# Performance work log

Measured on AMD Instinct MI355X. Metric: run time of the kernel, lower is better.

The kernel has to match this reference:

```python
import jax, jax.numpy as jnp
import numpy as np

HIDDEN = 2048
N_HEADS = 16
N_KV_GROUPS = 4
HEAD_DIM = HIDDEN // N_HEADS  # 128
LATENT = 512
KV_SIZE = HIDDEN * N_KV_GROUPS // N_HEADS  # 512


def setup_inputs() -> dict:
    key = jax.random.key(0)
    ks = jax.random.split(key, 11)
    s = 0.02
    return {
        "hidden_states": jax.random.normal(ks[0], (2, 2048, HIDDEN), dtype=jnp.float32),
        "Wq": jax.random.normal(ks[1], (HIDDEN, HIDDEN), dtype=jnp.float32) * s,
        "bq": jnp.zeros((HIDDEN,), dtype=jnp.float32),
        "Wl": jax.random.normal(ks[2], (HIDDEN, LATENT), dtype=jnp.float32) * s,
        "bl": jnp.zeros((LATENT,), dtype=jnp.float32),
        "Wk": jax.random.normal(ks[3], (LATENT, KV_SIZE), dtype=jnp.float32) * s,
        "bk": jnp.zeros((KV_SIZE,), dtype=jnp.float32),
        "Wv": jax.random.normal(ks[4], (LATENT, KV_SIZE), dtype=jnp.float32) * s,
        "bv": jnp.zeros((KV_SIZE,), dtype=jnp.float32),
        "Wo": jax.random.normal(ks[5], (HIDDEN, HIDDEN), dtype=jnp.float32) * s,
        "bo": jnp.zeros((HIDDEN,), dtype=jnp.float32),
    }


def reference(hidden_states, Wq, bq, Wl, bl, Wk, bk, Wv, bv, Wo, bo):
    B, S, _ = hidden_states.shape
    heads_per_group = N_HEADS // N_KV_GROUPS

    q = hidden_states @ Wq + bq                      # [B,S,H*D]
    latent = hidden_states @ Wl + bl                 # [B,S,L]
    k = latent @ Wk + bk                             # [B,S,G*D]
    v = latent @ Wv + bv

    q = q.reshape(B, S, N_HEADS, HEAD_DIM).transpose(0, 2, 1, 3)        # [B,H,S,D]
    k = k.reshape(B, S, N_KV_GROUPS, HEAD_DIM).transpose(0, 2, 1, 3)    # [B,G,S,D]
    v = v.reshape(B, S, N_KV_GROUPS, HEAD_DIM).transpose(0, 2, 1, 3)

    # repeat_interleave over head dim: group g -> heads [g*hpg, (g+1)*hpg)
    k = jnp.repeat(k, heads_per_group, axis=1)       # [B,H,S,D]
    v = jnp.repeat(v, heads_per_group, axis=1)

    scale = 1.0 / np.sqrt(HEAD_DIM).astype(np.float32)
    scores = jnp.einsum("bhqd,bhkd->bhqk", q, k) * scale
    probs = jax.nn.softmax(scores, axis=-1)          # dropout p=0 (eval) -> identity
    ctx = jnp.einsum("bhqk,bhkd->bhqd", probs, v)    # [B,H,S,D]
    ctx = ctx.transpose(0, 2, 1, 3).reshape(B, S, HIDDEN)
    return ctx @ Wo + bo
```

## Files before the change

### kernel.cpp

```cpp
#include <hip/hip_runtime.h>
#include <stdint.h>


#define DEV static __device__ __forceinline__

using short8 = __attribute__((ext_vector_type(8))) short;
using f32x4  = __attribute__((ext_vector_type(4))) float;

typedef __attribute__((address_space(1))) void gvoid;
typedef __attribute__((address_space(3))) void lvoid;

DEV unsigned short f2b(float f) {
  unsigned u = __builtin_bit_cast(unsigned, f);
  unsigned r = (u + 0x7fffu + ((u >> 16) & 1u)) >> 16;
  return (unsigned short)r;
}
DEV float b2f(unsigned short s) {
  unsigned u = ((unsigned)s) << 16;
  return __builtin_bit_cast(float, u);
}

DEV unsigned cvtpk(float lo, float hi) {
  unsigned r;
  asm("v_cvt_pk_bf16_f32 %0, %1, %2" : "=v"(r) : "v"(lo), "v"(hi));
  return r;
}

DEV float ex2(float x) { return __builtin_amdgcn_exp2f(x); }

DEV void async16(const void* g, void* l) {
  __builtin_amdgcn_global_load_lds((gvoid*)(uintptr_t)g,
                                   (lvoid*)(uint32_t)(uintptr_t)l, 16, 0, 0);
}

DEV f32x4 mfma16(short8 a, short8 b, f32x4 c) {
  return __builtin_amdgcn_mfma_f32_16x16x32_bf16(a, b, c, 0, 0, 0);
}

__global__ __launch_bounds__(256) void mega_prep(
    const float* __restrict__ h, unsigned short* __restrict__ hb,
    const float* __restrict__ Wq, const float* __restrict__ Wl,
    const float* __restrict__ Wk, const float* __restrict__ Wv,
    const float* __restrict__ Wo,
    unsigned short* __restrict__ WqlT, unsigned short* __restrict__ WkvT,
    unsigned short* __restrict__ WoT,
    const float* __restrict__ bq, const float* __restrict__ bl,
    const float* __restrict__ bk, const float* __restrict__ bv,
    float* __restrict__ bql, float* __restrict__ bkv, float qscale) {
  __shared__ float tile[32][33];
  const int bid = blockIdx.x;
  const int tid = threadIdx.x;

  if (bid < 4096) {
    long i = ((long)bid * 256 + tid) * 8;
    float4 a = *(const float4*)(h + i);
    float4 b = *(const float4*)(h + i + 4);
    short8 o;
    o[0] = (short)f2b(a.x); o[1] = (short)f2b(a.y);
    o[2] = (short)f2b(a.z); o[3] = (short)f2b(a.w);
    o[4] = (short)f2b(b.x); o[5] = (short)f2b(b.y);
    o[6] = (short)f2b(b.z); o[7] = (short)f2b(b.w);
    *(short8*)(hb + i) = o;
    return;
  }

  const float* in; unsigned short* out; int R, C, bx, by; float sc = 1.0f;
  if (bid < 8192) {
    int l = bid - 4096; in = Wq; out = WqlT; R = 2048; C = 2048;
    bx = l & 63; by = l >> 6; sc = qscale;
  } else if (bid < 9216) {
    int l = bid - 8192; in = Wl; out = WqlT + 2048 * 2048; R = 2048; C = 512;
    bx = l & 15; by = l >> 4;
  } else if (bid < 9472) {
    int l = bid - 9216; in = Wk; out = WkvT; R = 512; C = 512;
    bx = l & 15; by = l >> 4;
  } else if (bid < 9728) {
    int l = bid - 9472; in = Wv; out = WkvT + 262144; R = 512; C = 512;
    bx = l & 15; by = l >> 4;
  } else if (bid < 13824) {
    int l = bid - 9728; in = Wo; out = WoT; R = 2048; C = 2048;
    bx = l & 63; by = l >> 6;
  } else {
    for (int t = tid; t < 2560; t += 256)
      bql[t] = (t < 2048) ? bq[t] * qscale : bl[t - 2048];
    for (int t = tid; t < 1024; t += 256)
      bkv[t] = (t < 512) ? bk[t] : bv[t - 512];
    return;
  }

  int bc = bx * 32, br = by * 32;
  int tx = tid & 31, ty0 = tid >> 5;
#pragma unroll
  for (int ty = ty0; ty < 32; ty += 8)
    tile[ty][tx] = in[(size_t)(br + ty) * C + bc + tx] * sc;
  __syncthreads();
#pragma unroll
  for (int ty = ty0; ty < 32; ty += 8)
    out[(size_t)(bc + ty) * R + br + tx] = f2b(tile[tx][ty]);
}

__global__ __launch_bounds__(256) void transpose_v(
    const unsigned short* __restrict__ in, unsigned short* __restrict__ out) {
  __shared__ float tile[32][33];
  int b = blockIdx.z;
  int bc = blockIdx.x * 32;
  int br = blockIdx.y * 32;
  const unsigned short* ip = in + (size_t)b * 2048 * 1024 + 512;
  unsigned short* op = out + (size_t)b * 512 * 2048;
  int tx = threadIdx.x & 31, ty0 = threadIdx.x >> 5;
#pragma unroll
  for (int ty = ty0; ty < 32; ty += 8)
    tile[ty][tx] = b2f(ip[(size_t)(br + ty) * 1024 + bc + tx]);
  __syncthreads();
#pragma unroll
  for (int ty = ty0; ty < 32; ty += 8)
    op[(size_t)(bc + ty) * 2048 + br + tx] = f2b(tile[tx][ty]);
}

template <int OUT_F32>
__global__ __launch_bounds__(256) void gemm_bt(
    const unsigned short* __restrict__ A, const unsigned short* __restrict__ Bt,
    const float* __restrict__ bias, void* __restrict__ Cout,
    int M, int N, int K, int lda, float scale) {
  __shared__ unsigned short As[128 * 32];
  __shared__ unsigned short Bs[128 * 32];
  int tid = threadIdx.x;
  int lane = tid & 63, wave = tid >> 6;
  int wr = wave >> 1, wc = wave & 1;
  int lq = lane & 15, grp = lane >> 4;
  int brow = blockIdx.y * 128, bcol = blockIdx.x * 128;

  f32x4 acc[4][4] = {};

  for (int k0 = 0; k0 < K; k0 += 32) {
    {
      int e0 = tid * 8;
      int r0 = e0 >> 5, c0 = e0 & 31;
      async16(A + (size_t)(brow + r0) * lda + k0 + c0, As + e0);
      async16(Bt + (size_t)(bcol + r0) * K + k0 + c0, Bs + e0);
      int e1 = (256 + tid) * 8;
      int r1 = e1 >> 5, c1 = e1 & 31;
      async16(A + (size_t)(brow + r1) * lda + k0 + c1, As + e1);
      async16(Bt + (size_t)(bcol + r1) * K + k0 + c1, Bs + e1);
    }
    __syncthreads();

    short8 af[4], bf[4];
#pragma unroll
    for (int m = 0; m < 4; m++)
      af[m] = *(const short8*)(As + (wr * 64 + m * 16 + lq) * 32 + grp * 8);
#pragma unroll
    for (int n = 0; n < 4; n++)
      bf[n] = *(const short8*)(Bs + (wc * 64 + n * 16 + lq) * 32 + grp * 8);
#pragma unroll
    for (int m = 0; m < 4; m++)
#pragma unroll
      for (int n = 0; n < 4; n++)
        acc[m][n] = mfma16(af[m], bf[n], acc[m][n]);
    __syncthreads();
  }

#pragma unroll
  for (int n = 0; n < 4; n++) {
    int col = bcol + wc * 64 + n * 16 + lq;
    float bv = bias[col];
#pragma unroll
    for (int m = 0; m < 4; m++) {
#pragma unroll
      for (int r = 0; r < 4; r++) {
        int row = brow + wr * 64 + m * 16 + grp * 4 + r;
        float v = (acc[m][n][r] + bv) * scale;
        if (OUT_F32)
          ((float*)Cout)[(size_t)row * N + col] = v;
        else
          ((unsigned short*)Cout)[(size_t)row * N + col] = f2b(v);
      }
    }
  }
}

template <int OUT_F32>
__global__ __launch_bounds__(512, 1) void gemm_8ph(
    const unsigned short* __restrict__ A, const unsigned short* __restrict__ Bt,
    const float* __restrict__ bias, void* __restrict__ Cout,
    int M, int N, int K, float scale) {
  __shared__ __align__(1024) unsigned short L[2][32768];
  const int tid = threadIdx.x, lane = tid & 63, wave = tid >> 6;
  const int lq = lane & 15, grp = lane >> 4;
  const int wr = wave >> 2, wc = wave & 3;

  const int gx = gridDim.x;
  int nwg = gx * gridDim.y;
  int bid = blockIdx.y * gx + blockIdx.x;
  int wgid = (bid & 7) * (nwg >> 3) + (bid >> 3);
  int bx = wgid % gx, by = wgid / gx;
  const int brow = by * 256, bcol = bx * 256;

  const unsigned short* srcA[2];
  const unsigned short* srcB[2];
  unsigned short* dstA[2];
  unsigned short* dstB[2];
#pragma unroll
  for (int j = 0; j < 2; j++) {
    int f = wave + j * 8, kk = f & 1, fi = f >> 1;
    int awr = fi >> 2, aml = fi & 3;
    srcA[j] = A + (size_t)(brow + (awr * 8 + aml) * 16 + lq) * K + kk * 32 + grp * 8;
    dstA[j] = &L[0][0] + f * 512 + lane * 8;
    int bwc = fi >> 1, bnl = fi & 1;
    srcB[j] = Bt + (size_t)(bcol + (bwc * 4 + bnl) * 16 + lq) * K + kk * 32 + grp * 8;
    dstB[j] = &L[0][0] + 16384 + f * 512 + lane * 8;
  }
  auto stgA = [&](int p, int mh, int k0) {
#pragma unroll
    for (int j = 0; j < 2; j++)
      async16(srcA[j] + (size_t)mh * 64 * K + k0, dstA[j] + p * 32768 + mh * 8192);
  };
  auto stgB = [&](int p, int nh, int k0) {
#pragma unroll
    for (int j = 0; j < 2; j++)
      async16(srcB[j] + (size_t)nh * 32 * K + k0, dstB[j] + p * 32768 + nh * 8192);
  };
  auto ldAf = [&](int p, int mh, int ml, int kk) -> short8 {
    return *(const short8*)(&L[0][0] + p * 32768 + mh * 8192 +
                            ((wr * 4 + ml) * 2 + kk) * 512 + lane * 8);
  };
  auto ldBf = [&](int p, int nh, int nl, int kk) -> short8 {
    return *(const short8*)(&L[0][0] + p * 32768 + 16384 + nh * 8192 +
                            ((wc * 2 + nl) * 2 + kk) * 512 + lane * 8);
  };

  f32x4 acc[8][4] = {};
  short8 af[4][2], bf0[2][2], bf1[2][2];
  const int NT = K >> 6;

  stgA(0, 0, 0); stgB(0, 0, 0); stgB(0, 1, 0); stgA(0, 1, 0);
  asm volatile("s_waitcnt vmcnt(4)" ::: "memory");
  __builtin_amdgcn_s_barrier();

  for (int T = 0; T < NT; ++T) {
    const int cur = T & 1, nxt = cur ^ 1;
    const bool pf = (T + 1 < NT);
    const int k1 = (T + 1) << 6;

#pragma unroll
    for (int ml = 0; ml < 4; ml++) {
      af[ml][0] = ldAf(cur, 0, ml, 0);
      af[ml][1] = ldAf(cur, 0, ml, 1);
    }
#pragma unroll
    for (int nl = 0; nl < 2; nl++) {
      bf0[nl][0] = ldBf(cur, 0, nl, 0);
      bf0[nl][1] = ldBf(cur, 0, nl, 1);
    }
    if (pf) stgA(nxt, 0, k1);
    __builtin_amdgcn_s_setprio(1);
#pragma unroll
    for (int ml = 0; ml < 4; ml++)
#pragma unroll
      for (int nl = 0; nl < 2; nl++) {
        acc[ml][nl] = mfma16(af[ml][0], bf0[nl][0], acc[ml][nl]);
        acc[ml][nl] = mfma16(af[ml][1], bf0[nl][1], acc[ml][nl]);
      }
    __builtin_amdgcn_s_setprio(0);
    if (pf) asm volatile("s_waitcnt vmcnt(4)" ::: "memory");
    else    asm volatile("s_waitcnt vmcnt(2)" ::: "memory");
    __builtin_amdgcn_s_barrier();

#pragma unroll
    for (int nl = 0; nl < 2; nl++) {
      bf1[nl][0] = ldBf(cur, 1, nl, 0);
      bf1[nl][1] = ldBf(cur, 1, nl, 1);
    }
    if (pf) stgB(nxt, 0, k1);
    __builtin_amdgcn_s_setprio(1);
#pragma unroll
    for (int ml = 0; ml < 4; ml++)
#pragma unroll
      for (int nl = 0; nl < 2; nl++) {
        acc[ml][2 + nl] = mfma16(af[ml][0], bf1[nl][0], acc[ml][2 + nl]);
        acc[ml][2 + nl] = mfma16(af[ml][1], bf1[nl][1], acc[ml][2 + nl]);
      }
    __builtin_amdgcn_s_setprio(0);
    if (pf) asm volatile("s_waitcnt vmcnt(4)" ::: "memory");
    else    asm volatile("s_waitcnt vmcnt(0)" ::: "memory");
    __builtin_amdgcn_s_barrier();

#pragma unroll
    for (int ml = 0; ml < 4; ml++) {
      af[ml][0] = ldAf(cur, 1, ml, 0);
      af[ml][1] = ldAf(cur, 1, ml, 1);
    }
    if (pf) stgB(nxt, 1, k1);
    __builtin_amdgcn_s_setprio(1);
#pragma unroll
    for (int ml = 0; ml < 4; ml++)
#pragma unroll
      for (int nl = 0; nl < 2; nl++) {
        acc[4 + ml][nl] = mfma16(af[ml][0], bf0[nl][0], acc[4 + ml][nl]);
        acc[4 + ml][nl] = mfma16(af[ml][1], bf0[nl][1], acc[4 + ml][nl]);
      }
    __builtin_amdgcn_s_setprio(0);
    __builtin_amdgcn_s_barrier();

    if (pf) stgA(nxt, 1, k1);
    __builtin_amdgcn_s_setprio(1);
#pragma unroll
    for (int ml = 0; ml < 4; ml++)
#pragma unroll
      for (int nl = 0; nl < 2; nl++) {
        acc[4 + ml][2 + nl] = mfma16(af[ml][0], bf1[nl][0], acc[4 + ml][2 + nl]);
        acc[4 + ml][2 + nl] = mfma16(af[ml][1], bf1[nl][1], acc[4 + ml][2 + nl]);
      }
    __builtin_amdgcn_s_setprio(0);
    if (pf) asm volatile("s_waitcnt vmcnt(4)" ::: "memory");
    __builtin_amdgcn_s_barrier();
  }

#pragma unroll
  for (int mh = 0; mh < 2; mh++)
#pragma unroll
    for (int ml = 0; ml < 4; ml++)
#pragma unroll
      for (int nh = 0; nh < 2; nh++)
#pragma unroll
        for (int nl = 0; nl < 2; nl++) {
          int col = bcol + wc * 64 + (nh * 2 + nl) * 16 + lq;
          float bv = bias[col];
          f32x4 a = acc[mh * 4 + ml][nh * 2 + nl];
#pragma unroll
          for (int r = 0; r < 4; r++) {
            int row = brow + wr * 128 + (mh * 4 + ml) * 16 + grp * 4 + r;
            float v = (a[r] + bv) * scale;
            if (OUT_F32)
              ((float*)Cout)[(size_t)row * N + col] = v;
            else
              ((unsigned short*)Cout)[(size_t)row * N + col] = f2b(v);
          }
        }
}

__global__ __launch_bounds__(256, 2) void attn_kernel(
    const unsigned short* __restrict__ q,
    const unsigned short* __restrict__ kv,
    const unsigned short* __restrict__ vt,
    unsigned short* __restrict__ ctx) {
  __shared__ unsigned short KV[2][32][512];
  const int lane = threadIdx.x & 63, wave = threadIdx.x >> 6;
  const int lq = lane & 15, grp = lane >> 4;
  const int bid = blockIdx.x;
  const int combo = bid & 7;
  const int slot = bid >> 3;
  const int b = combo >> 2, g = combo & 3;
  const int h = g * 4 + (slot >> 4);
  const int qbase = (slot & 15) * 128 + wave * 32;

  short8 qf[2][4];
#pragma unroll
  for (int qs = 0; qs < 2; qs++) {
    const unsigned short* qp =
        q + ((size_t)(b * 2048 + qbase + qs * 16 + lq)) * 2560 + h * 128 + grp * 8;
#pragma unroll
    for (int c = 0; c < 4; c++) qf[qs][c] = *(const short8*)(qp + c * 32);
  }

  f32x4 o[2][8] = {};
  float lsum[2] = {0.f, 0.f};
  const float C = 20.0f;

  const int kvperm = (lq >> 2) * 8 + (lq & 3);
  const unsigned short* kB = kv + (size_t)b * 2048 * 1024 + g * 128 + grp * 8;
  const unsigned short* vB =
      vt + ((size_t)((b * 4 + g) * 128 + lq)) * 2048 + grp * 8;
  const int fbase = wave * 8;
  unsigned short* dstb = &KV[0][fbase][0] + lane * 8;

  auto stage = [&](int bn, int kv0) {
    unsigned short* dst = dstb + bn * 16384;
    if (fbase < 16) {
#pragma unroll
      for (int j = 0; j < 8; j++) {
        int f = fbase + j, t = f >> 2, c = f & 3;
        const unsigned short* src =
            kB + (size_t)(kv0 + (t >> 1) * 32 + (t & 1) * 4 + kvperm) * 1024 + c * 32;
        async16(src, dst + j * 512);
      }
    } else {
#pragma unroll
      for (int j = 0; j < 8; j++) {
        int f = fbase - 16 + j, d0 = f >> 1, u = f & 1;
        const unsigned short* src = vB + (size_t)(d0 * 16) * 2048 + kv0 + u * 32;
        async16(src, dst + j * 512);
      }
    }
  };

  stage(0, 0);
  int buf = 0;
  for (int it = 0; it < 32; ++it) {
    __syncthreads();
    if (it < 31) stage(buf ^ 1, (it + 1) * 64);
    const unsigned short* Kb = &KV[buf][0][0] + lane * 8;

    f32x4 s[2][4] = {};
    __builtin_amdgcn_s_setprio(1);
#pragma unroll
    for (int c = 0; c < 4; c++) {
      short8 kf0 = *(const short8*)(Kb + (0 + c) * 512);
      short8 kf1 = *(const short8*)(Kb + (4 + c) * 512);
      short8 kf2 = *(const short8*)(Kb + (8 + c) * 512);
      short8 kf3 = *(const short8*)(Kb + (12 + c) * 512);
#pragma unroll
      for (int qs = 0; qs < 2; qs++) {
        s[qs][0] = mfma16(kf0, qf[qs][c], s[qs][0]);
        s[qs][1] = mfma16(kf1, qf[qs][c], s[qs][1]);
        s[qs][2] = mfma16(kf2, qf[qs][c], s[qs][2]);
        s[qs][3] = mfma16(kf3, qf[qs][c], s[qs][3]);
      }
    }
    __builtin_amdgcn_s_setprio(0);

    short8 pf[2][2];
#pragma unroll
    for (int qs = 0; qs < 2; qs++) {
      float ps = 0.f;
      union { short8 v; unsigned w[4]; } pk0, pk1;
#pragma unroll
      for (int t = 0; t < 4; t++) {
        float e0 = ex2(s[qs][t][0] - C);
        float e1 = ex2(s[qs][t][1] - C);
        float e2 = ex2(s[qs][t][2] - C);
        float e3 = ex2(s[qs][t][3] - C);
        ps += (e0 + e1) + (e2 + e3);
        unsigned w0 = cvtpk(e0, e1), w1 = cvtpk(e2, e3);
        if (t == 0) { pk0.w[0] = w0; pk0.w[1] = w1; }
        else if (t == 1) { pk0.w[2] = w0; pk0.w[3] = w1; }
        else if (t == 2) { pk1.w[0] = w0; pk1.w[1] = w1; }
        else { pk1.w[2] = w0; pk1.w[3] = w1; }
      }
      lsum[qs] += ps;
      pf[qs][0] = pk0.v;
      pf[qs][1] = pk1.v;
    }

    const unsigned short* Vb = Kb + 16 * 512;
    __builtin_amdgcn_s_setprio(1);
#pragma unroll
    for (int d0 = 0; d0 < 8; d0++) {
      short8 v0 = *(const short8*)(Vb + (d0 * 2 + 0) * 512);
      short8 v1 = *(const short8*)(Vb + (d0 * 2 + 1) * 512);
#pragma unroll
      for (int qs = 0; qs < 2; qs++) {
        o[qs][d0] = mfma16(pf[qs][0], v0, o[qs][d0]);
        o[qs][d0] = mfma16(pf[qs][1], v1, o[qs][d0]);
      }
    }
    __builtin_amdgcn_s_setprio(0);
    buf ^= 1;
  }

  unsigned short* cp = ctx + ((size_t)(b * 2048 + qbase)) * 2048 + h * 128;
#pragma unroll
  for (int qs = 0; qs < 2; qs++) {
    float l = lsum[qs];
    l += __shfl_xor(l, 16);
    l += __shfl_xor(l, 32);
    float ri = 1.0f / l;
    float r0 = __shfl(ri, grp * 4 + 0), r1 = __shfl(ri, grp * 4 + 1);
    float r2 = __shfl(ri, grp * 4 + 2), r3 = __shfl(ri, grp * 4 + 3);
#pragma unroll
    for (int d0 = 0; d0 < 8; d0++) {
      int col = d0 * 16 + lq;
      cp[(size_t)(qs * 16 + grp * 4 + 0) * 2048 + col] = f2b(o[qs][d0][0] * r0);
      cp[(size_t)(qs * 16 + grp * 4 + 1) * 2048 + col] = f2b(o[qs][d0][1] * r1);
      cp[(size_t)(qs * 16 + grp * 4 + 2) * 2048 + col] = f2b(o[qs][d0][2] * r2);
      cp[(size_t)(qs * 16 + grp * 4 + 3) * 2048 + col] = f2b(o[qs][d0][3] * r3);
    }
  }
}

extern "C" void kernel_launch(void* const* d_in, const int* in_sizes, int n_in,
                              void* d_out, int out_size, void* d_ws, size_t ws_size,
                              hipStream_t stream) {
  const float* h  = (const float*)d_in[0];
  const float* Wq = (const float*)d_in[1];
  const float* bq = (const float*)d_in[2];
  const float* Wl = (const float*)d_in[3];
  const float* bl = (const float*)d_in[4];
  const float* Wk = (const float*)d_in[5];
  const float* bk = (const float*)d_in[6];
  const float* Wv = (const float*)d_in[7];
  const float* bv = (const float*)d_in[8];
  const float* Wo = (const float*)d_in[9];
  const float* bo = (const float*)d_in[10];
  float* out = (float*)d_out;

  const int M = 4096;

  char* w = (char*)d_ws;
  auto take = [&](size_t elems) {
    void* p = (void*)w;
    w += (elems * 2 + 255) & ~(size_t)255;
    return (unsigned short*)p;
  };
  unsigned short* hb   = take(8388608);
  unsigned short* WqlT = take(5242880);
  unsigned short* WkvT = take(524288);
  unsigned short* WoT  = take(4194304);
  unsigned short* qlat = take(10485760);
  unsigned short* kvb  = take(4194304);
  unsigned short* vtb  = take(2097152);
  unsigned short* ctx  = take(8388608);
  float* bql = (float*)take(2560);
  float* bkv = (float*)take(1024);

  const float scale = 0.08838834764831845f * 1.4426950408889634f;

  mega_prep<<<13825, 256, 0, stream>>>(h, hb, Wq, Wl, Wk, Wv, Wo,
                                       WqlT, WkvT, WoT,
                                       bq, bl, bk, bv, bql, bkv, scale);

  gemm_8ph<0><<<dim3(10, 16), 512, 0, stream>>>(hb, WqlT, bql, qlat, M, 2560, 2048, 1.0f);
  gemm_bt<0><<<dim3(8, 32), 256, 0, stream>>>(qlat + 2048, WkvT, bkv, kvb, M, 1024, 512, 2560, 1.0f);

  transpose_v<<<dim3(16, 64, 2), 256, 0, stream>>>(kvb, vtb);

  attn_kernel<<<512, 256, 0, stream>>>(qlat, kvb, vtb, ctx);

  gemm_8ph<1><<<dim3(8, 16), 512, 0, stream>>>(ctx, WoT, bo, out, M, 2048, 2048, 1.0f);
}
```

Before: 241.5 us.

## Split fused Q/latent GEMM and switch to 256x128 two-phase GEMM tiles

Replaces the 256x256 eight-phase GEMM with a 256x128 tile kernel using two B sub-phases, giving 256 workgroups instead of 160/128 for the Q and output projections. The fused Q+latent projection is split into a separate Q GEMM and a latent GEMM run by the smaller gemm_bt kernel, so buffers and bias layouts change (q row stride becomes 2048). The goal is better CU fill on the 256-CU device, at the cost of lower per-tile reuse and one extra kernel launch.

```diff
diff --git a/kernel.cpp b/kernel.cpp
--- a/kernel.cpp
+++ b/kernel.cpp
@@ -42,11 +42,11 @@
     const float* __restrict__ Wq, const float* __restrict__ Wl,
     const float* __restrict__ Wk, const float* __restrict__ Wv,
     const float* __restrict__ Wo,
-    unsigned short* __restrict__ WqlT, unsigned short* __restrict__ WkvT,
-    unsigned short* __restrict__ WoT,
-    const float* __restrict__ bq, const float* __restrict__ bl,
+    unsigned short* __restrict__ WqT, unsigned short* __restrict__ WlT,
+    unsigned short* __restrict__ WkvT, unsigned short* __restrict__ WoT,
+    const float* __restrict__ bq,
     const float* __restrict__ bk, const float* __restrict__ bv,
-    float* __restrict__ bql, float* __restrict__ bkv, float qscale) {
+    float* __restrict__ bqs, float* __restrict__ bkv, float qscale) {
   __shared__ float tile[32][33];
   const int bid = blockIdx.x;
   const int tid = threadIdx.x;
@@ -66,10 +66,10 @@
 
   const float* in; unsigned short* out; int R, C, bx, by; float sc = 1.0f;
   if (bid < 8192) {
-    int l = bid - 4096; in = Wq; out = WqlT; R = 2048; C = 2048;
+    int l = bid - 4096; in = Wq; out = WqT; R = 2048; C = 2048;
     bx = l & 63; by = l >> 6; sc = qscale;
   } else if (bid < 9216) {
-    int l = bid - 8192; in = Wl; out = WqlT + 2048 * 2048; R = 2048; C = 512;
+    int l = bid - 8192; in = Wl; out = WlT; R = 2048; C = 512;
     bx = l & 15; by = l >> 4;
   } else if (bid < 9472) {
     int l = bid - 9216; in = Wk; out = WkvT; R = 512; C = 512;
@@ -81,8 +81,7 @@
     int l = bid - 9728; in = Wo; out = WoT; R = 2048; C = 2048;
     bx = l & 63; by = l >> 6;
   } else {
-    for (int t = tid; t < 2560; t += 256)
-      bql[t] = (t < 2048) ? bq[t] * qscale : bl[t - 2048];
+    for (int t = tid; t < 2048; t += 256) bqs[t] = bq[t] * qscale;
     for (int t = tid; t < 1024; t += 256)
       bkv[t] = (t < 512) ? bk[t] : bv[t - 512];
     return;
@@ -180,61 +179,59 @@
 }
 
 template <int OUT_F32>
-__global__ __launch_bounds__(512, 1) void gemm_8ph(
+__global__ __launch_bounds__(512, 1) void gemm_2ph(
     const unsigned short* __restrict__ A, const unsigned short* __restrict__ Bt,
     const float* __restrict__ bias, void* __restrict__ Cout,
     int M, int N, int K, float scale) {
-  __shared__ __align__(1024) unsigned short L[2][32768];
+  __shared__ __align__(1024) unsigned short L[2][24576];
   const int tid = threadIdx.x, lane = tid & 63, wave = tid >> 6;
   const int lq = lane & 15, grp = lane >> 4;
-  const int wr = wave >> 2, wc = wave & 3;
+  const int wr = wave >> 1, wc = wave & 1;
 
   const int gx = gridDim.x;
   int nwg = gx * gridDim.y;
   int bid = blockIdx.y * gx + blockIdx.x;
   int wgid = (bid & 7) * (nwg >> 3) + (bid >> 3);
   int bx = wgid % gx, by = wgid / gx;
-  const int brow = by * 256, bcol = bx * 256;
-
-  const unsigned short* srcA[2];
-  const unsigned short* srcB[2];
-  unsigned short* dstA[2];
-  unsigned short* dstB[2];
-#pragma unroll
-  for (int j = 0; j < 2; j++) {
-    int f = wave + j * 8, kk = f & 1, fi = f >> 1;
-    int awr = fi >> 2, aml = fi & 3;
-    srcA[j] = A + (size_t)(brow + (awr * 8 + aml) * 16 + lq) * K + kk * 32 + grp * 8;
-    dstA[j] = &L[0][0] + f * 512 + lane * 8;
-    int bwc = fi >> 1, bnl = fi & 1;
-    srcB[j] = Bt + (size_t)(bcol + (bwc * 4 + bnl) * 16 + lq) * K + kk * 32 + grp * 8;
-    dstB[j] = &L[0][0] + 16384 + f * 512 + lane * 8;
-  }
-  auto stgA = [&](int p, int mh, int k0) {
-#pragma unroll
-    for (int j = 0; j < 2; j++)
-      async16(srcA[j] + (size_t)mh * 64 * K + k0, dstA[j] + p * 32768 + mh * 8192);
-  };
-  auto stgB = [&](int p, int nh, int k0) {
-#pragma unroll
-    for (int j = 0; j < 2; j++)
-      async16(srcB[j] + (size_t)nh * 32 * K + k0, dstB[j] + p * 32768 + nh * 8192);
-  };
-  auto ldAf = [&](int p, int mh, int ml, int kk) -> short8 {
-    return *(const short8*)(&L[0][0] + p * 32768 + mh * 8192 +
-                            ((wr * 4 + ml) * 2 + kk) * 512 + lane * 8);
-  };
-  auto ldBf = [&](int p, int nh, int nl, int kk) -> short8 {
-    return *(const short8*)(&L[0][0] + p * 32768 + 16384 + nh * 8192 +
-                            ((wc * 2 + nl) * 2 + kk) * 512 + lane * 8);
-  };
-
-  f32x4 acc[8][4] = {};
-  short8 af[4][2], bf0[2][2], bf1[2][2];
+  const int brow = by * 256, bcol = bx * 128;
+
+  const unsigned short* srcA[4];
+  unsigned short* dstA[4];
+#pragma unroll
+  for (int j = 0; j < 4; j++) {
+    int fa = wave * 4 + j;
+    srcA[j] = A + (size_t)(brow + (fa >> 1) * 16 + lq) * K + (fa & 1) * 32 + grp * 8;
+    dstA[j] = &L[0][0] + fa * 512 + lane * 8;
+  }
+  const int g0 = (wave & 3) | ((wave >> 2) << 3), g1 = g0 + 4;
+  const unsigned short* srcB0 =
+      Bt + (size_t)(bcol + (g0 >> 1) * 16 + lq) * K + (g0 & 1) * 32 + grp * 8;
+  const unsigned short* srcB1 =
+      Bt + (size_t)(bcol + (g1 >> 1) * 16 + lq) * K + (g1 & 1) * 32 + grp * 8;
+  unsigned short* dstB0 = &L[0][0] + 16384 + g0 * 512 + lane * 8;
+  unsigned short* dstB1 = &L[0][0] + 16384 + g1 * 512 + lane * 8;
+
+  auto stgA = [&](int p, int k0) {
+#pragma unroll
+    for (int j = 0; j < 4; j++) async16(srcA[j] + k0, dstA[j] + p * 24576);
+  };
+  auto stgB = [&](int p, int k0) {
+    async16(srcB0 + k0, dstB0 + p * 24576);
+    async16(srcB1 + k0, dstB1 + p * 24576);
+  };
+  auto ldAf = [&](int p, int ml, int kk) -> short8 {
+    return *(const short8*)(&L[p][((wr * 4 + ml) * 2 + kk) * 512 + lane * 8]);
+  };
+  auto ldBf = [&](int p, int nl, int kk) -> short8 {
+    return *(const short8*)(&L[p][16384 + ((wc * 4 + nl) * 2 + kk) * 512 + lane * 8]);
+  };
+
+  f32x4 acc[4][4] = {};
+  short8 af[4][2], bf[2][2];
   const int NT = K >> 6;
 
-  stgA(0, 0, 0); stgB(0, 0, 0); stgB(0, 1, 0); stgA(0, 1, 0);
-  asm volatile("s_waitcnt vmcnt(4)" ::: "memory");
+  stgA(0, 0); stgB(0, 0);
+  asm volatile("s_waitcnt vmcnt(1)" ::: "memory");
   __builtin_amdgcn_s_barrier();
 
   for (int T = 0; T < NT; ++T) {
@@ -244,41 +241,22 @@
 
 #pragma unroll
     for (int ml = 0; ml < 4; ml++) {
-      af[ml][0] = ldAf(cur, 0, ml, 0);
-      af[ml][1] = ldAf(cur, 0, ml, 1);
+      af[ml][0] = ldAf(cur, ml, 0);
+      af[ml][1] = ldAf(cur, ml, 1);
     }
 #pragma unroll
     for (int nl = 0; nl < 2; nl++) {
-      bf0[nl][0] = ldBf(cur, 0, nl, 0);
-      bf0[nl][1] = ldBf(cur, 0, nl, 1);
-    }
-    if (pf) stgA(nxt, 0, k1);
+      bf[nl][0] = ldBf(cur, nl, 0);
+      bf[nl][1] = ldBf(cur, nl, 1);
+    }
+    if (pf) stgA(nxt, k1);
     __builtin_amdgcn_s_setprio(1);
 #pragma unroll
     for (int ml = 0; ml < 4; ml++)
 #pragma unroll
       for (int nl = 0; nl < 2; nl++) {
-        acc[ml][nl] = mfma16(af[ml][0], bf0[nl][0], acc[ml][nl]);
-        acc[ml][nl] = mfma16(af[ml][1], bf0[nl][1], acc[ml][nl]);
-      }
-    __builtin_amdgcn_s_setprio(0);
-    if (pf) asm volatile("s_waitcnt vmcnt(4)" ::: "memory");
-    else    asm volatile("s_waitcnt vmcnt(2)" ::: "memory");
-    __builtin_amdgcn_s_barrier();
-
-#pragma unroll
-    for (int nl = 0; nl < 2; nl++) {
-      bf1[nl][0] = ldBf(cur, 1, nl, 0);
-      bf1[nl][1] = ldBf(cur, 1, nl, 1);
-    }
-    if (pf) stgB(nxt, 0, k1);
-    __builtin_amdgcn_s_setprio(1);
-#pragma unroll
-    for (int ml = 0; ml < 4; ml++)
-#pragma unroll
-      for (int nl = 0; nl < 2; nl++) {
-        acc[ml][2 + nl] = mfma16(af[ml][0], bf1[nl][0], acc[ml][2 + nl]);
-        acc[ml][2 + nl] = mfma16(af[ml][1], bf1[nl][1], acc[ml][2 + nl]);
+        acc[ml][nl] = mfma16(af[ml][0], bf[nl][0], acc[ml][nl]);
+        acc[ml][nl] = mfma16(af[ml][1], bf[nl][1], acc[ml][nl]);
       }
     __builtin_amdgcn_s_setprio(0);
     if (pf) asm volatile("s_waitcnt vmcnt(4)" ::: "memory");
@@ -286,57 +264,41 @@
     __builtin_amdgcn_s_barrier();
 
 #pragma unroll
+    for (int nl = 0; nl < 2; nl++) {
+      bf[nl][0] = ldBf(cur, 2 + nl, 0);
+      bf[nl][1] = ldBf(cur, 2 + nl, 1);
+    }
+    if (pf) stgB(nxt, k1);
+    __builtin_amdgcn_s_setprio(1);
+#pragma unroll
+    for (int ml = 0; ml < 4; ml++)
+#pragma unroll
+      for (int nl = 0; nl < 2; nl++) {
+        acc[ml][2 + nl] = mfma16(af[ml][0], bf[nl][0], acc[ml][2 + nl]);
+        acc[ml][2 + nl] = mfma16(af[ml][1], bf[nl][1], acc[ml][2 + nl]);
+      }
+    __builtin_amdgcn_s_setprio(0);
+    if (pf) asm volatile("s_waitcnt vmcnt(1)" ::: "memory");
+    __builtin_amdgcn_s_barrier();
+  }
+
+#pragma unroll
+  for (int nl = 0; nl < 4; nl++) {
+    int col = bcol + wc * 64 + nl * 16 + lq;
+    float bv = bias[col];
+#pragma unroll
     for (int ml = 0; ml < 4; ml++) {
-      af[ml][0] = ldAf(cur, 1, ml, 0);
-      af[ml][1] = ldAf(cur, 1, ml, 1);
-    }
-    if (pf) stgB(nxt, 1, k1);
-    __builtin_amdgcn_s_setprio(1);
-#pragma unroll
-    for (int ml = 0; ml < 4; ml++)
-#pragma unroll
-      for (int nl = 0; nl < 2; nl++) {
-        acc[4 + ml][nl] = mfma16(af[ml][0], bf0[nl][0], acc[4 + ml][nl]);
-        acc[4 + ml][nl] = mfma16(af[ml][1], bf0[nl][1], acc[4 + ml][nl]);
-      }
-    __builtin_amdgcn_s_setprio(0);
-    __builtin_amdgcn_s_barrier();
-
-    if (pf) stgA(nxt, 1, k1);
-    __builtin_amdgcn_s_setprio(1);
-#pragma unroll
-    for (int ml = 0; ml < 4; ml++)
-#pragma unroll
-      for (int nl = 0; nl < 2; nl++) {
-        acc[4 + ml][2 + nl] = mfma16(af[ml][0], bf1[nl][0], acc[4 + ml][2 + nl]);
-        acc[4 + ml][2 + nl] = mfma16(af[ml][1], bf1[nl][1], acc[4 + ml][2 + nl]);
-      }
-    __builtin_amdgcn_s_setprio(0);
-    if (pf) asm volatile("s_waitcnt vmcnt(4)" ::: "memory");
-    __builtin_amdgcn_s_barrier();
-  }
-
-#pragma unroll
-  for (int mh = 0; mh < 2; mh++)
-#pragma unroll
-    for (int ml = 0; ml < 4; ml++)
-#pragma unroll
-      for (int nh = 0; nh < 2; nh++)
-#pragma unroll
-        for (int nl = 0; nl < 2; nl++) {
-          int col = bcol + wc * 64 + (nh * 2 + nl) * 16 + lq;
-          float bv = bias[col];
-          f32x4 a = acc[mh * 4 + ml][nh * 2 + nl];
-#pragma unroll
-          for (int r = 0; r < 4; r++) {
-            int row = brow + wr * 128 + (mh * 4 + ml) * 16 + grp * 4 + r;
-            float v = (a[r] + bv) * scale;
-            if (OUT_F32)
-              ((float*)Cout)[(size_t)row * N + col] = v;
-            else
-              ((unsigned short*)Cout)[(size_t)row * N + col] = f2b(v);
-          }
-        }
+#pragma unroll
+      for (int r = 0; r < 4; r++) {
+        int row = brow + wr * 64 + ml * 16 + grp * 4 + r;
+        float v = (acc[ml][nl][r] + bv) * scale;
+        if (OUT_F32)
+          ((float*)Cout)[(size_t)row * N + col] = v;
+        else
+          ((unsigned short*)Cout)[(size_t)row * N + col] = f2b(v);
+      }
+    }
+  }
 }
 
 __global__ __launch_bounds__(256, 2) void attn_kernel(
@@ -358,7 +320,7 @@
 #pragma unroll
   for (int qs = 0; qs < 2; qs++) {
     const unsigned short* qp =
-        q + ((size_t)(b * 2048 + qbase + qs * 16 + lq)) * 2560 + h * 128 + grp * 8;
+        q + ((size_t)(b * 2048 + qbase + qs * 16 + lq)) * 2048 + h * 128 + grp * 8;
 #pragma unroll
     for (int c = 0; c < 4; c++) qf[qs][c] = *(const short8*)(qp + c * 32);
   }
@@ -503,28 +465,31 @@
     return (unsigned short*)p;
   };
   unsigned short* hb   = take(8388608);
-  unsigned short* WqlT = take(5242880);
+  unsigned short* WqT  = take(4194304);
+  unsigned short* WlT  = take(1048576);
   unsigned short* WkvT = take(524288);
   unsigned short* WoT  = take(4194304);
-  unsigned short* qlat = take(10485760);
+  unsigned short* qb   = take(8388608);
+  unsigned short* lat  = take(2097152);
   unsigned short* kvb  = take(4194304);
   unsigned short* vtb  = take(2097152);
   unsigned short* ctx  = take(8388608);
-  float* bql = (float*)take(2560);
-  float* bkv = (float*)take(1024);
+  float* bqs = (float*)take(4096);
+  float* bkv = (float*)take(2048);
 
   const float scale = 0.08838834764831845f * 1.4426950408889634f;
 
   mega_prep<<<13825, 256, 0, stream>>>(h, hb, Wq, Wl, Wk, Wv, Wo,
-                                       WqlT, WkvT, WoT,
-                                       bq, bl, bk, bv, bql, bkv, scale);
-
-  gemm_8ph<0><<<dim3(10, 16), 512, 0, stream>>>(hb, WqlT, bql, qlat, M, 2560, 2048, 1.0f);
-  gemm_bt<0><<<dim3(8, 32), 256, 0, stream>>>(qlat + 2048, WkvT, bkv, kvb, M, 1024, 512, 2560, 1.0f);
+                                       WqT, WlT, WkvT, WoT,
+                                       bq, bk, bv, bqs, bkv, scale);
+
+  gemm_2ph<0><<<dim3(16, 16), 512, 0, stream>>>(hb, WqT, bqs, qb, M, 2048, 2048, 1.0f);
+  gemm_bt<0><<<dim3(4, 32), 256, 0, stream>>>(hb, WlT, bl, lat, M, 512, 2048, 2048, 1.0f);
+  gemm_bt<0><<<dim3(8, 32), 256, 0, stream>>>(lat, WkvT, bkv, kvb, M, 1024, 512, 512, 1.0f);
 
   transpose_v<<<dim3(16, 64, 2), 256, 0, stream>>>(kvb, vtb);
 
-  attn_kernel<<<512, 256, 0, stream>>>(qlat, kvb, vtb, ctx);
-
-  gemm_8ph<1><<<dim3(8, 16), 512, 0, stream>>>(ctx, WoT, bo, out, M, 2048, 2048, 1.0f);
-}
+  attn_kernel<<<512, 256, 0, stream>>>(qb, kvb, vtb, ctx);
+
+  gemm_2ph<1><<<dim3(16, 16), 512, 0, stream>>>(ctx, WoT, bo, out, M, 2048, 2048, 1.0f);
+}
```

New measurement: 272.9 us. 1.13x slower.
